# Kernel optimization log

Hardware: AMD Instinct MI355X
Metric: run time of the kernel (lower is better)

Reference implementation:

```python
import jax, jax.numpy as jnp
from jax import lax
import numpy as np

B, D, P, C = 16384, 256, 512, 20  # batch, input_dim, prototype_dim, n_class


def setup_inputs() -> dict:
    key = jax.random.key(0)
    k1, k2, k3 = jax.random.split(key, 3)
    return {
        "inputs": jax.random.normal(k1, (B, D), dtype=jnp.float32),
        "W": jax.random.normal(k2, (P, D), dtype=jnp.float32),
        "BETA": jax.random.normal(k3, (P, C), dtype=jnp.float32),
        "alpha": jnp.zeros((P, 1), dtype=jnp.float32),
        "gamma": jnp.full((P, 1), 0.1, dtype=jnp.float32),
        "n_class": C,
        "prototype_dim": P,
    }


def reference(inputs, W, BETA, alpha, gamma, n_class, prototype_dim):
    # inputs: [B, D], W: [P, D], BETA: [P, C], alpha/gamma: [P, 1]
    BETA2 = BETA * BETA
    U = BETA2 / BETA2.sum(axis=1, keepdims=True)          # [P, C]
    alphap = 0.99 / (1.0 + jnp.exp(-alpha))               # [P, 1]
    # d[k, b] = 0.5 * ||x_b - W_k||^2 via the expanded quadratic form
    d = 0.5 * (jnp.sum(W * W, axis=1)[:, None]
               + jnp.sum(inputs * inputs, axis=1)[None, :]
               - 2.0 * W @ inputs.T)                      # [P, B]
    expo = jnp.exp(-(gamma * gamma) * d)                  # [P, B]
    s = alphap * expo                                     # [P, B]

    bsz = inputs.shape[0]

    def step(mk, xs):
        # mk: [C+1, B] combined mass; xs = (U_k [C], s_k [B])
        Uk, sk = xs
        m_c = Uk[:, None] * sk[None, :]                   # [C, B] singleton masses
        m_n = 1.0 - sk                                    # [B]   mass on ignorance
        mk_c, mk_n = mk[:-1], mk[-1]
        new_c = mk_c * (m_c + m_n[None, :]) + m_c * mk_n[None, :]
        new_n = mk_n * m_n
        return jnp.concatenate([new_c, new_n[None, :]], axis=0), None

    mk0 = jnp.concatenate([jnp.zeros((n_class, bsz), dtype=inputs.dtype),
                           jnp.ones((1, bsz), dtype=inputs.dtype)], axis=0)
    mk, _ = lax.scan(step, mk0, (U, s))                   # sequential over P prototypes
    K = mk.sum(axis=0)                                    # [B]
    return (mk / K[None, :]).T                            # [B, C+1]
```

## Files before the change

### kernel.cpp

```cpp
#include <hip/hip_runtime.h>
#include <math.h>


#define NBATCH 16384
#define ND     256
#define NP     512
#define NCLS   20
#define OC     21

typedef short  short8  __attribute__((ext_vector_type(8)));
typedef short  short4v __attribute__((ext_vector_type(4)));
typedef unsigned short ushort8 __attribute__((ext_vector_type(8)));
typedef float  f32x16  __attribute__((ext_vector_type(16)));

#define OFF_PWH 0u
#define OFF_PWL 262144u
#define OFF_VS  524288u
#define OFF_WQ  567296u
#define OFF_AP  569344u
#define OFF_G2  571392u

__device__ __forceinline__ unsigned short f2bf_rn(float f) {
  unsigned int u = __float_as_uint(f);
  unsigned int r = (u + 0x7FFFu + ((u >> 16) & 1u)) >> 16;
  return (unsigned short)r;
}
__device__ __forceinline__ float bf2f(unsigned short h) {
  return __uint_as_float(((unsigned int)h) << 16);
}

__global__ __launch_bounds__(256)
void prep(const float* __restrict__ Wsrc, const float* __restrict__ BETA,
          const float* __restrict__ alpha, const float* __restrict__ gamma,
          unsigned short* __restrict__ dh, unsigned short* __restrict__ dl,
          float* __restrict__ sq, float* __restrict__ VS,
          float* __restrict__ AP, float* __restrict__ G2)
{
  const int bid = blockIdx.x;
  if (bid < 64) {
    const int tid = bid * 256 + threadIdx.x;
    const int row = tid >> 5, seg = tid & 31;
    const float4* s4 = (const float4*)(Wsrc + (size_t)row * ND + seg * 8);
    const float4 a = s4[0], b = s4[1];
    const float v[8] = {a.x, a.y, a.z, a.w, b.x, b.y, b.z, b.w};
    ushort8 hv, lv;
    float ssq = 0.f;
    #pragma unroll
    for (int j = 0; j < 8; ++j) {
      ssq = fmaf(v[j], v[j], ssq);
      const unsigned short hh = f2bf_rn(v[j]);
      hv[j] = hh;
      lv[j] = f2bf_rn(v[j] - bf2f(hh));
    }
    const int tile = row >> 5, m = row & 31, step = seg >> 1, r = seg & 1;
    const size_t cidx = (size_t)(tile * 16 + step) * 64 + m + 32 * r;
    *(ushort8*)(dh + cidx * 8) = hv;
    *(ushort8*)(dl + cidx * 8) = lv;
    #pragma unroll
    for (int off = 1; off < 32; off <<= 1) ssq += __shfl_xor(ssq, off, 64);
    if (seg == 0) sq[row] = ssq;
  } else {
    const int k = (bid - 64) * 256 + threadIdx.x;
    if (k >= NP) return;
    float bv[NCLS], bs = 0.f;
    #pragma unroll
    for (int c = 0; c < NCLS; ++c) { bv[c] = BETA[k * NCLS + c]; bs = fmaf(bv[c], bv[c], bs); }
    const float binv = 1.f / bs;
    #pragma unroll
    for (int c = 0; c < NCLS; ++c) VS[c * NP + k] = 1.f - bv[c] * bv[c] * binv;
    VS[NCLS * NP + k] = 1.f;
    AP[k] = 0.99f / (1.f + __expf(-alpha[k]));
    const float g = gamma[k];
    G2[k] = g * g;
  }
}

__device__ __forceinline__ void mfma_pass8(
    const short* __restrict__ Ah, const short* __restrict__ Al,
    const short8* __restrict__ bHc, const short8* __restrict__ bLc,
    const int lane, const int sh, const float* __restrict__ xqs,
    const float wqk, const float apk, const float g2k, float* __restrict__ sout)
{
  short8 wbh[8], wbl[8];
  #pragma unroll
  for (int p = 0; p < 8; ++p) { wbh[p] = bHc[p * 64]; wbl[p] = bLc[p * 64]; }

  f32x16 accA, accB;
  #pragma unroll
  for (int i = 0; i < 16; ++i) { accA[i] = 0.f; accB[i] = 0.f; }
  const short8* aH = (const short8*)Ah + (size_t)sh * 1024 + lane;
  const short8* aL = (const short8*)Al + (size_t)sh * 1024 + lane;
  #pragma unroll
  for (int step = 0; step < 16; ++step) {
    const short8 ah = aH[step * 64], al = aL[step * 64];
    const short8 bh = wbh[step & 7], bl = wbl[step & 7];
    if (step < 8) {
      wbh[step & 7] = bHc[(step + 8) * 64];
      wbl[step & 7] = bLc[(step + 8) * 64];
    }
    accA = __builtin_amdgcn_mfma_f32_32x32x16_bf16(ah, bh, accA, 0, 0, 0);
    accB = __builtin_amdgcn_mfma_f32_32x32x16_bf16(ah, bl, accB, 0, 0, 0);
    accB = __builtin_amdgcn_mfma_f32_32x32x16_bf16(al, bh, accB, 0, 0, 0);
  }
  const int h = lane >> 5;
  #pragma unroll
  for (int rg = 0; rg < 16; ++rg) {
    const int   m  = (rg & 3) + 8 * (rg >> 2) + 4 * h;
    const float dv = 0.5f * (wqk + xqs[sh * 32 + m]) - (accA[rg] + accB[rg]);
    sout[rg] = apk * __expf(-g2k * dv);
  }
}

__global__ __launch_bounds__(512)
void evid64(const float* __restrict__ X,
            const unsigned short* __restrict__ PWH, const unsigned short* __restrict__ PWL,
            const float* __restrict__ VS, const float* __restrict__ WQ,
            const float* __restrict__ AP, const float* __restrict__ G2,
            float* __restrict__ OUT)
{
  __shared__ __align__(16) char pool[131072];
  __shared__ float vsl[8 * NCLS * 32];
  __shared__ float xqs[64];
  short* Ah = (short*)pool;
  short* Al = (short*)(pool + 32768);
  float* sc = (float*)(pool + 65536);

  const int t    = threadIdx.x;
  const int lane = t & 63;
  const int wv   = __builtin_amdgcn_readfirstlane(t >> 6);
  const int bx   = blockIdx.x;
  const int bbase = bx * 64;
  const int pl = lane & 31, h = lane >> 5;

  {
    const int r  = t >> 3;
    const int sg = t & 7;
    const int rsh = r >> 5, rm = r & 31;
    const float* xrow = X + (size_t)(bbase + r) * ND;
    float ssq = 0.f;
    #pragma unroll
    for (int it = 0; it < 8; ++it) {
      const int c0 = it * 32 + sg * 4;
      const float4 v = *(const float4*)(xrow + c0);
      const float vv[4] = {v.x, v.y, v.z, v.w};
      short4v h4, l4;
      #pragma unroll
      for (int j = 0; j < 4; ++j) {
        ssq = fmaf(vv[j], vv[j], ssq);
        const unsigned short hh = f2bf_rn(vv[j]);
        h4[j] = (short)hh;
        l4[j] = (short)f2bf_rn(vv[j] - bf2f(hh));
      }
      const int step = c0 >> 4, hf = (c0 >> 3) & 1, j0 = c0 & 7;
      const int base = (((rsh * 16 + step) * 64) + (rm + 32 * hf)) * 8 + j0;
      *(short4v*)&Ah[base] = h4;
      *(short4v*)&Al[base] = l4;
    }
    ssq += __shfl_xor(ssq, 1, 64);
    ssq += __shfl_xor(ssq, 2, 64);
    ssq += __shfl_xor(ssq, 4, 64);
    if (sg == 0) xqs[r] = ssq;
  }
  __syncthreads();

  float Apc[OC];
  #pragma unroll
  for (int c = 0; c < OC; ++c) Apc[c] = 1.0f;

  float* vw = vsl + wv * (NCLS * 32);

  #pragma unroll
  for (int ph = 0; ph < 2; ++ph) {
    {
      const float* vg = VS + ph * 256 + wv * 32;
      #pragma unroll
      for (int i = 0; i < 10; ++i) {
        const int idx = i * 64 + lane;
        vw[idx] = vg[(idx >> 5) * NP + (idx & 31)];
      }
    }

    const int kp = ph * 256 + wv * 32 + pl;
    const float wqk = WQ[kp], apk = AP[kp], g2k = G2[kp];
    const short8* bHc = (const short8*)PWH + (size_t)(ph * 8 + wv) * 1024 + lane;
    const short8* bLc = (const short8*)PWL + (size_t)(ph * 8 + wv) * 1024 + lane;
    const int p = wv * 32 + pl;

    #pragma unroll
    for (int sh = 0; sh < 2; ++sh) {
      float sreg[16];
      mfma_pass8(Ah, Al, bHc, bLc, lane, sh, xqs, wqk, apk, g2k, sreg);
      #pragma unroll
      for (int rg = 0; rg < 16; ++rg) {
        const int m = (rg & 3) + 8 * (rg >> 2) + 4 * h;
        const int b = sh * 32 + m;
        sc[b * 256 + ((p + 4 * b) & 255)] = sreg[rg];
      }
    }

    {
      float sv[32];
      const int c0 = (wv * 32 + 4 * lane);
      #pragma unroll
      for (int q = 0; q < 8; ++q)
        *(float4*)&sv[4 * q] = *(const float4*)&sc[lane * 256 + ((c0 + 4 * q) & 255)];

      #pragma unroll 4
      for (int c = 0; c < NCLS; ++c) {
        const float* vp = vw + c * 32;
        float f8[8];
        #pragma unroll
        for (int j = 0; j < 8; ++j) f8[j] = fmaf(-sv[j], vp[j], 1.0f);
        #pragma unroll
        for (int j = 8; j < 32; ++j) f8[j & 7] *= fmaf(-sv[j], vp[j], 1.0f);
        Apc[c] *= ((f8[0] * f8[1]) * (f8[2] * f8[3])) *
                  ((f8[4] * f8[5]) * (f8[6] * f8[7]));
      }
      {
        float f8[8];
        #pragma unroll
        for (int j = 0; j < 8; ++j) f8[j] = 1.0f - sv[j];
        #pragma unroll
        for (int j = 8; j < 32; ++j) f8[j & 7] *= (1.0f - sv[j]);
        Apc[NCLS] *= ((f8[0] * f8[1]) * (f8[2] * f8[3])) *
                     ((f8[4] * f8[5]) * (f8[6] * f8[7]));
      }
    }
  }
  __syncthreads();

  float* E  = (float*)pool;
  float* R  = (float*)(pool + 43008);
  float* kv = (float*)(pool + 48384);
  #pragma unroll
  for (int c = 0; c < OC; ++c) E[(wv * OC + c) * 64 + lane] = Apc[c];
  __syncthreads();
  {
    const int b = t & 63, j = t >> 6;
    for (int c = j; c < OC; c += 8) {
      float p = E[c * 64 + b];
      #pragma unroll
      for (int w = 1; w < 8; ++w) p *= E[(w * OC + c) * 64 + b];
      R[c * 64 + b] = p;
    }
  }
  __syncthreads();
  if (t < 64) {
    const float Nv = R[NCLS * 64 + t];
    float K = Nv;
    #pragma unroll
    for (int c = 0; c < NCLS; ++c) K += R[c * 64 + t] - Nv;
    kv[t] = 1.0f / K;
  }
  __syncthreads();
  for (int idx = t; idx < 64 * OC; idx += 512) {
    const int b = idx / OC, c = idx - b * OC;
    const float Nv = R[NCLS * 64 + b];
    const float ik = kv[b];
    OUT[(size_t)bx * 64 * OC + idx] = (c < NCLS) ? (R[c * 64 + b] - Nv) * ik : Nv * ik;
  }
}

extern "C" void kernel_launch(void* const* d_in, const int* in_sizes, int n_in,
                              void* d_out, int out_size, void* d_ws, size_t ws_size,
                              hipStream_t stream) {
  (void)in_sizes; (void)n_in; (void)out_size; (void)ws_size;
  const float* X     = (const float*)d_in[0];
  const float* Wm    = (const float*)d_in[1];
  const float* BETA  = (const float*)d_in[2];
  const float* ALPHA = (const float*)d_in[3];
  const float* GAMMA = (const float*)d_in[4];
  float* OUT = (float*)d_out;

  char* ws = (char*)d_ws;
  unsigned short* PWH = (unsigned short*)(ws + OFF_PWH);
  unsigned short* PWL = (unsigned short*)(ws + OFF_PWL);
  float* VS = (float*)(ws + OFF_VS);
  float* WQ = (float*)(ws + OFF_WQ);
  float* AP = (float*)(ws + OFF_AP);
  float* G2 = (float*)(ws + OFF_G2);

  hipLaunchKernelGGL(prep, dim3(66), dim3(256), 0, stream,
                     Wm, BETA, ALPHA, GAMMA, PWH, PWL, WQ, VS, AP, G2);
  hipLaunchKernelGGL(evid64, dim3(NBATCH / 64), dim3(512), 0, stream,
                     X, PWH, PWL, VS, WQ, AP, G2, OUT);
}
```

Measured before the change: 97.82 us.

## Double wavefronts per block, splitting batch halves and prototype halves across waves

The block grows from 8 to 16 wavefronts. Each wave pair now shares a prototype slice, and each wave handles one batch half (sh) instead of looping over both. The per-lane combination loop is split into two 16-prototype halves, which are merged with a cross-half shuffle before the block reduction. This aims to raise latency hiding and occupancy within the 128KB LDS-limited single block per CU. The cost is an extra barrier per phase, a shallower B-operand prefetch, and a tighter register budget under waves_per_eu(4,4).

Result: slower. 119.3 us (+22.0%).

```diff
diff --git a/kernel.cpp b/kernel.cpp
--- a/kernel.cpp
+++ b/kernel.cpp
@@ -75,15 +75,15 @@
   }
 }
 
-__device__ __forceinline__ void mfma_pass8(
+__device__ __forceinline__ void mfma_pass4(
     const short* __restrict__ Ah, const short* __restrict__ Al,
     const short8* __restrict__ bHc, const short8* __restrict__ bLc,
     const int lane, const int sh, const float* __restrict__ xqs,
     const float wqk, const float apk, const float g2k, float* __restrict__ sout)
 {
-  short8 wbh[8], wbl[8];
-  #pragma unroll
-  for (int p = 0; p < 8; ++p) { wbh[p] = bHc[p * 64]; wbl[p] = bLc[p * 64]; }
+  short8 wbh[4], wbl[4];
+  #pragma unroll
+  for (int p = 0; p < 4; ++p) { wbh[p] = bHc[p * 64]; wbl[p] = bLc[p * 64]; }
 
   f32x16 accA, accB;
   #pragma unroll
@@ -93,10 +93,10 @@
   #pragma unroll
   for (int step = 0; step < 16; ++step) {
     const short8 ah = aH[step * 64], al = aL[step * 64];
-    const short8 bh = wbh[step & 7], bl = wbl[step & 7];
-    if (step < 8) {
-      wbh[step & 7] = bHc[(step + 8) * 64];
-      wbl[step & 7] = bLc[(step + 8) * 64];
+    const short8 bh = wbh[step & 3], bl = wbl[step & 3];
+    if (step < 12) {
+      wbh[step & 3] = bHc[(step + 4) * 64];
+      wbl[step & 3] = bLc[(step + 4) * 64];
     }
     accA = __builtin_amdgcn_mfma_f32_32x32x16_bf16(ah, bh, accA, 0, 0, 0);
     accB = __builtin_amdgcn_mfma_f32_32x32x16_bf16(ah, bl, accB, 0, 0, 0);
@@ -111,12 +111,12 @@
   }
 }
 
-__global__ __launch_bounds__(512)
-void evid64(const float* __restrict__ X,
-            const unsigned short* __restrict__ PWH, const unsigned short* __restrict__ PWL,
-            const float* __restrict__ VS, const float* __restrict__ WQ,
-            const float* __restrict__ AP, const float* __restrict__ G2,
-            float* __restrict__ OUT)
+__global__ __launch_bounds__(1024) __attribute__((amdgpu_waves_per_eu(4, 4)))
+void evid64w(const float* __restrict__ X,
+             const unsigned short* __restrict__ PWH, const unsigned short* __restrict__ PWL,
+             const float* __restrict__ VS, const float* __restrict__ WQ,
+             const float* __restrict__ AP, const float* __restrict__ G2,
+             float* __restrict__ OUT)
 {
   __shared__ __align__(16) char pool[131072];
   __shared__ float vsl[8 * NCLS * 32];
@@ -127,20 +127,22 @@
 
   const int t    = threadIdx.x;
   const int lane = t & 63;
-  const int wv   = __builtin_amdgcn_readfirstlane(t >> 6);
+  const int w    = __builtin_amdgcn_readfirstlane(t >> 6);
+  const int i    = w >> 1;
+  const int s    = w & 1;
   const int bx   = blockIdx.x;
   const int bbase = bx * 64;
   const int pl = lane & 31, h = lane >> 5;
 
   {
-    const int r  = t >> 3;
-    const int sg = t & 7;
+    const int r  = t >> 4;
+    const int sg = t & 15;
     const int rsh = r >> 5, rm = r & 31;
     const float* xrow = X + (size_t)(bbase + r) * ND;
     float ssq = 0.f;
     #pragma unroll
-    for (int it = 0; it < 8; ++it) {
-      const int c0 = it * 32 + sg * 4;
+    for (int it = 0; it < 4; ++it) {
+      const int c0 = it * 64 + sg * 4;
       const float4 v = *(const float4*)(xrow + c0);
       const float vv[4] = {v.x, v.y, v.z, v.w};
       short4v h4, l4;
@@ -159,6 +161,7 @@
     ssq += __shfl_xor(ssq, 1, 64);
     ssq += __shfl_xor(ssq, 2, 64);
     ssq += __shfl_xor(ssq, 4, 64);
+    ssq += __shfl_xor(ssq, 8, 64);
     if (sg == 0) xqs[r] = ssq;
   }
   __syncthreads();
@@ -167,80 +170,88 @@
   #pragma unroll
   for (int c = 0; c < OC; ++c) Apc[c] = 1.0f;
 
-  float* vw = vsl + wv * (NCLS * 32);
+  float* vw = vsl + i * (NCLS * 32);
 
   #pragma unroll
   for (int ph = 0; ph < 2; ++ph) {
+    if (ph == 1) __syncthreads();
+
     {
-      const float* vg = VS + ph * 256 + wv * 32;
-      #pragma unroll
-      for (int i = 0; i < 10; ++i) {
-        const int idx = i * 64 + lane;
+      const float* vg = VS + ph * 256 + i * 32;
+      #pragma unroll
+      for (int q = 0; q < 10; ++q) {
+        const int idx = q * 64 + lane;
         vw[idx] = vg[(idx >> 5) * NP + (idx & 31)];
       }
     }
 
-    const int kp = ph * 256 + wv * 32 + pl;
+    const int kp = ph * 256 + i * 32 + pl;
     const float wqk = WQ[kp], apk = AP[kp], g2k = G2[kp];
-    const short8* bHc = (const short8*)PWH + (size_t)(ph * 8 + wv) * 1024 + lane;
-    const short8* bLc = (const short8*)PWL + (size_t)(ph * 8 + wv) * 1024 + lane;
-    const int p = wv * 32 + pl;
-
-    #pragma unroll
-    for (int sh = 0; sh < 2; ++sh) {
-      float sreg[16];
-      mfma_pass8(Ah, Al, bHc, bLc, lane, sh, xqs, wqk, apk, g2k, sreg);
+    const short8* bHc = (const short8*)PWH + (size_t)(ph * 8 + i) * 1024 + lane;
+    const short8* bLc = (const short8*)PWL + (size_t)(ph * 8 + i) * 1024 + lane;
+
+    float sreg[16];
+    mfma_pass4(Ah, Al, bHc, bLc, lane, s, xqs, wqk, apk, g2k, sreg);
+
+    {
+      const int p = i * 32 + pl;
       #pragma unroll
       for (int rg = 0; rg < 16; ++rg) {
         const int m = (rg & 3) + 8 * (rg >> 2) + 4 * h;
-        const int b = sh * 32 + m;
+        const int b = s * 32 + m;
         sc[b * 256 + ((p + 4 * b) & 255)] = sreg[rg];
       }
     }
 
     {
-      float sv[32];
-      const int c0 = (wv * 32 + 4 * lane);
-      #pragma unroll
-      for (int q = 0; q < 8; ++q)
-        *(float4*)&sv[4 * q] = *(const float4*)&sc[lane * 256 + ((c0 + 4 * q) & 255)];
-
+      const int b = s * 32 + pl;
+      float sv[16];
+      const int cb = i * 32 + h * 16 + 4 * b;
+      #pragma unroll
+      for (int q = 0; q < 4; ++q)
+        *(float4*)&sv[4 * q] = *(const float4*)&sc[b * 256 + ((cb + 4 * q) & 255)];
+
+      const float* vb = vw + h * 16;
       #pragma unroll 4
       for (int c = 0; c < NCLS; ++c) {
-        const float* vp = vw + c * 32;
-        float f8[8];
-        #pragma unroll
-        for (int j = 0; j < 8; ++j) f8[j] = fmaf(-sv[j], vp[j], 1.0f);
-        #pragma unroll
-        for (int j = 8; j < 32; ++j) f8[j & 7] *= fmaf(-sv[j], vp[j], 1.0f);
-        Apc[c] *= ((f8[0] * f8[1]) * (f8[2] * f8[3])) *
-                  ((f8[4] * f8[5]) * (f8[6] * f8[7]));
+        const float* vp = vb + c * 32;
+        float f4[4];
+        #pragma unroll
+        for (int j = 0; j < 4; ++j) f4[j] = fmaf(-sv[j], vp[j], 1.0f);
+        #pragma unroll
+        for (int j = 4; j < 16; ++j) f4[j & 3] *= fmaf(-sv[j], vp[j], 1.0f);
+        Apc[c] *= (f4[0] * f4[1]) * (f4[2] * f4[3]);
       }
       {
-        float f8[8];
-        #pragma unroll
-        for (int j = 0; j < 8; ++j) f8[j] = 1.0f - sv[j];
-        #pragma unroll
-        for (int j = 8; j < 32; ++j) f8[j & 7] *= (1.0f - sv[j]);
-        Apc[NCLS] *= ((f8[0] * f8[1]) * (f8[2] * f8[3])) *
-                     ((f8[4] * f8[5]) * (f8[6] * f8[7]));
-      }
-    }
-  }
+        float f4[4];
+        #pragma unroll
+        for (int j = 0; j < 4; ++j) f4[j] = 1.0f - sv[j];
+        #pragma unroll
+        for (int j = 4; j < 16; ++j) f4[j & 3] *= (1.0f - sv[j]);
+        Apc[NCLS] *= (f4[0] * f4[1]) * (f4[2] * f4[3]);
+      }
+    }
+  }
+  #pragma unroll
+  for (int c = 0; c < OC; ++c) Apc[c] *= __shfl_xor(Apc[c], 32, 64);
+
   __syncthreads();
 
   float* E  = (float*)pool;
   float* R  = (float*)(pool + 43008);
   float* kv = (float*)(pool + 48384);
-  #pragma unroll
-  for (int c = 0; c < OC; ++c) E[(wv * OC + c) * 64 + lane] = Apc[c];
+  if (h == 0) {
+    const int b = s * 32 + pl;
+    #pragma unroll
+    for (int c = 0; c < OC; ++c) E[(i * OC + c) * 64 + b] = Apc[c];
+  }
   __syncthreads();
   {
     const int b = t & 63, j = t >> 6;
-    for (int c = j; c < OC; c += 8) {
+    for (int c = j; c < OC; c += 16) {
       float p = E[c * 64 + b];
       #pragma unroll
-      for (int w = 1; w < 8; ++w) p *= E[(w * OC + c) * 64 + b];
+      for (int ww = 1; ww < 8; ++ww) p *= E[(ww * OC + c) * 64 + b];
       R[c * 64 + b] = p;
     }
   }
@@ -253,7 +264,7 @@
     kv[t] = 1.0f / K;
   }
   __syncthreads();
-  for (int idx = t; idx < 64 * OC; idx += 512) {
+  for (int idx = t; idx < 64 * OC; idx += 1024) {
     const int b = idx / OC, c = idx - b * OC;
     const float Nv = R[NCLS * 64 + b];
     const float ik = kv[b];
@@ -282,6 +293,6 @@
 
   hipLaunchKernelGGL(prep, dim3(66), dim3(256), 0, stream,
                      Wm, BETA, ALPHA, GAMMA, PWH, PWL, WQ, VS, AP, G2);
-  hipLaunchKernelGGL(evid64, dim3(NBATCH / 64), dim3(512), 0, stream,
+  hipLaunchKernelGGL(evid64w, dim3(NBATCH / 64), dim3(1024), 0, stream,
                      X, PWH, PWL, VS, WQ, AP, G2, OUT);
 }
```

## Fuse prototype preprocessing into main kernel and drop separate prep launch

Applied to the files above, without the earlier changes.

Removes the prep kernel and computes the W bf16 hi/lo split, the W row norms, the normalized BETA terms, alphap and gamma^2 inside each block of the main kernel, reading raw fp32 W directly. This removes one kernel launch and the workspace round trip along with the dependency between the two kernels. In exchange every one of the 256 blocks redoes the W conversion and reads twice as many bytes of W (fp32 instead of two bf16 arrays), adding VALU work in the MFMA loop. The W reads mostly hit L2.

Result: slower. 139.4 us (+42.5%).

```diff
diff --git a/kernel.cpp b/kernel.cpp
--- a/kernel.cpp
+++ b/kernel.cpp
@@ -10,15 +10,7 @@
 
 typedef short  short8  __attribute__((ext_vector_type(8)));
 typedef short  short4v __attribute__((ext_vector_type(4)));
-typedef unsigned short ushort8 __attribute__((ext_vector_type(8)));
 typedef float  f32x16  __attribute__((ext_vector_type(16)));
-
-#define OFF_PWH 0u
-#define OFF_PWL 262144u
-#define OFF_VS  524288u
-#define OFF_WQ  567296u
-#define OFF_AP  569344u
-#define OFF_G2  571392u
 
 __device__ __forceinline__ unsigned short f2bf_rn(float f) {
   unsigned int u = __float_as_uint(f);
@@ -29,94 +21,64 @@
   return __uint_as_float(((unsigned int)h) << 16);
 }
 
-__global__ __launch_bounds__(256)
-void prep(const float* __restrict__ Wsrc, const float* __restrict__ BETA,
-          const float* __restrict__ alpha, const float* __restrict__ gamma,
-          unsigned short* __restrict__ dh, unsigned short* __restrict__ dl,
-          float* __restrict__ sq, float* __restrict__ VS,
-          float* __restrict__ AP, float* __restrict__ G2)
+template<bool WQCOMP>
+__device__ __forceinline__ void mfma_pass_raw(
+    const short* __restrict__ Ah, const short* __restrict__ Al,
+    const float* __restrict__ bp,
+    const int lane, const int sh, const float* __restrict__ xqs,
+    float& wq, const float apk, const float g2k, float* __restrict__ sout)
 {
-  const int bid = blockIdx.x;
-  if (bid < 64) {
-    const int tid = bid * 256 + threadIdx.x;
-    const int row = tid >> 5, seg = tid & 31;
-    const float4* s4 = (const float4*)(Wsrc + (size_t)row * ND + seg * 8);
-    const float4 a = s4[0], b = s4[1];
-    const float v[8] = {a.x, a.y, a.z, a.w, b.x, b.y, b.z, b.w};
-    ushort8 hv, lv;
-    float ssq = 0.f;
-    #pragma unroll
-    for (int j = 0; j < 8; ++j) {
-      ssq = fmaf(v[j], v[j], ssq);
-      const unsigned short hh = f2bf_rn(v[j]);
-      hv[j] = hh;
-      lv[j] = f2bf_rn(v[j] - bf2f(hh));
-    }
-    const int tile = row >> 5, m = row & 31, step = seg >> 1, r = seg & 1;
-    const size_t cidx = (size_t)(tile * 16 + step) * 64 + m + 32 * r;
-    *(ushort8*)(dh + cidx * 8) = hv;
-    *(ushort8*)(dl + cidx * 8) = lv;
-    #pragma unroll
-    for (int off = 1; off < 32; off <<= 1) ssq += __shfl_xor(ssq, off, 64);
-    if (seg == 0) sq[row] = ssq;
-  } else {
-    const int k = (bid - 64) * 256 + threadIdx.x;
-    if (k >= NP) return;
-    float bv[NCLS], bs = 0.f;
-    #pragma unroll
-    for (int c = 0; c < NCLS; ++c) { bv[c] = BETA[k * NCLS + c]; bs = fmaf(bv[c], bv[c], bs); }
-    const float binv = 1.f / bs;
-    #pragma unroll
-    for (int c = 0; c < NCLS; ++c) VS[c * NP + k] = 1.f - bv[c] * bv[c] * binv;
-    VS[NCLS * NP + k] = 1.f;
-    AP[k] = 0.99f / (1.f + __expf(-alpha[k]));
-    const float g = gamma[k];
-    G2[k] = g * g;
-  }
-}
-
-__device__ __forceinline__ void mfma_pass8(
-    const short* __restrict__ Ah, const short* __restrict__ Al,
-    const short8* __restrict__ bHc, const short8* __restrict__ bLc,
-    const int lane, const int sh, const float* __restrict__ xqs,
-    const float wqk, const float apk, const float g2k, float* __restrict__ sout)
-{
-  short8 wbh[8], wbl[8];
-  #pragma unroll
-  for (int p = 0; p < 8; ++p) { wbh[p] = bHc[p * 64]; wbl[p] = bLc[p * 64]; }
+  float4 r0[4], r1[4];
+  #pragma unroll
+  for (int p = 0; p < 4; ++p) {
+    r0[p] = *(const float4*)(bp + p * 16);
+    r1[p] = *(const float4*)(bp + p * 16 + 4);
+  }
 
   f32x16 accA, accB;
   #pragma unroll
   for (int i = 0; i < 16; ++i) { accA[i] = 0.f; accB[i] = 0.f; }
   const short8* aH = (const short8*)Ah + (size_t)sh * 1024 + lane;
   const short8* aL = (const short8*)Al + (size_t)sh * 1024 + lane;
+  float ssq = 0.f;
   #pragma unroll
   for (int step = 0; step < 16; ++step) {
+    const float4 f0 = r0[step & 3], f1 = r1[step & 3];
+    if (step < 12) {
+      r0[step & 3] = *(const float4*)(bp + (step + 4) * 16);
+      r1[step & 3] = *(const float4*)(bp + (step + 4) * 16 + 4);
+    }
     const short8 ah = aH[step * 64], al = aL[step * 64];
-    const short8 bh = wbh[step & 7], bl = wbl[step & 7];
-    if (step < 8) {
-      wbh[step & 7] = bHc[(step + 8) * 64];
-      wbl[step & 7] = bLc[(step + 8) * 64];
+    const float v[8] = {f0.x, f0.y, f0.z, f0.w, f1.x, f1.y, f1.z, f1.w};
+    short8 bh, bl;
+    #pragma unroll
+    for (int j = 0; j < 8; ++j) {
+      if (WQCOMP) ssq = fmaf(v[j], v[j], ssq);
+      const unsigned short hh = f2bf_rn(v[j]);
+      bh[j] = (short)hh;
+      bl[j] = (short)f2bf_rn(v[j] - bf2f(hh));
     }
     accA = __builtin_amdgcn_mfma_f32_32x32x16_bf16(ah, bh, accA, 0, 0, 0);
     accB = __builtin_amdgcn_mfma_f32_32x32x16_bf16(ah, bl, accB, 0, 0, 0);
     accB = __builtin_amdgcn_mfma_f32_32x32x16_bf16(al, bh, accB, 0, 0, 0);
   }
+  if (WQCOMP) {
+    ssq += __shfl_xor(ssq, 32, 64);
+    wq = ssq;
+  }
   const int h = lane >> 5;
   #pragma unroll
   for (int rg = 0; rg < 16; ++rg) {
     const int   m  = (rg & 3) + 8 * (rg >> 2) + 4 * h;
-    const float dv = 0.5f * (wqk + xqs[sh * 32 + m]) - (accA[rg] + accB[rg]);
+    const float dv = 0.5f * (wq + xqs[sh * 32 + m]) - (accA[rg] + accB[rg]);
     sout[rg] = apk * __expf(-g2k * dv);
   }
 }
 
 __global__ __launch_bounds__(512)
-void evid64(const float* __restrict__ X,
-            const unsigned short* __restrict__ PWH, const unsigned short* __restrict__ PWL,
-            const float* __restrict__ VS, const float* __restrict__ WQ,
-            const float* __restrict__ AP, const float* __restrict__ G2,
-            float* __restrict__ OUT)
+void evid_one(const float* __restrict__ X,   const float* __restrict__ Wm,
+              const float* __restrict__ BETA, const float* __restrict__ ALPHA,
+              const float* __restrict__ GAMMA, float* __restrict__ OUT)
 {
   __shared__ __align__(16) char pool[131072];
   __shared__ float vsl[8 * NCLS * 32];
@@ -171,30 +133,43 @@
 
   #pragma unroll
   for (int ph = 0; ph < 2; ++ph) {
+    const int p0 = ph * 256 + wv * 32;
+
     {
-      const float* vg = VS + ph * 256 + wv * 32;
-      #pragma unroll
-      for (int i = 0; i < 10; ++i) {
-        const int idx = i * 64 + lane;
-        vw[idx] = vg[(idx >> 5) * NP + (idx & 31)];
-      }
-    }
-
-    const int kp = ph * 256 + wv * 32 + pl;
-    const float wqk = WQ[kp], apk = AP[kp], g2k = G2[kp];
-    const short8* bHc = (const short8*)PWH + (size_t)(ph * 8 + wv) * 1024 + lane;
-    const short8* bLc = (const short8*)PWL + (size_t)(ph * 8 + wv) * 1024 + lane;
-    const int p = wv * 32 + pl;
-
-    #pragma unroll
-    for (int sh = 0; sh < 2; ++sh) {
-      float sreg[16];
-      mfma_pass8(Ah, Al, bHc, bLc, lane, sh, xqs, wqk, apk, g2k, sreg);
+      const float* brow = BETA + (size_t)(p0 + pl) * NCLS + h * 10;
+      float b[10];
+      #pragma unroll
+      for (int q = 0; q < 10; ++q) b[q] = brow[q];
+      float bs = 0.f;
+      #pragma unroll
+      for (int q = 0; q < 10; ++q) bs = fmaf(b[q], b[q], bs);
+      bs += __shfl_xor(bs, 32, 64);
+      const float binv = 1.f / bs;
+      #pragma unroll
+      for (int q = 0; q < 10; ++q)
+        vw[(h * 10 + q) * 32 + pl] = 1.f - b[q] * b[q] * binv;
+    }
+
+    const int kp = p0 + pl;
+    const float apk = 0.99f / (1.f + __expf(-ALPHA[kp]));
+    const float gk  = GAMMA[kp];
+    const float g2k = gk * gk;
+
+    const float* bp = Wm + ((size_t)(ph * 8 + wv) * 32 + pl) * ND + h * 8;
+
+    float wq;
+    float sreg0[16], sreg1[16];
+    mfma_pass_raw<true >(Ah, Al, bp, lane, 0, xqs, wq, apk, g2k, sreg0);
+    mfma_pass_raw<false>(Ah, Al, bp, lane, 1, xqs, wq, apk, g2k, sreg1);
+
+    {
+      const int p = wv * 32 + pl;
       #pragma unroll
       for (int rg = 0; rg < 16; ++rg) {
         const int m = (rg & 3) + 8 * (rg >> 2) + 4 * h;
-        const int b = sh * 32 + m;
-        sc[b * 256 + ((p + 4 * b) & 255)] = sreg[rg];
+        sc[m * 256 + ((p + 4 * m) & 255)] = sreg0[rg];
+        const int b1 = m + 32;
+        sc[b1 * 256 + ((p + 4 * b1) & 255)] = sreg1[rg];
       }
     }
 
@@ -264,7 +239,7 @@
 extern "C" void kernel_launch(void* const* d_in, const int* in_sizes, int n_in,
                               void* d_out, int out_size, void* d_ws, size_t ws_size,
                               hipStream_t stream) {
-  (void)in_sizes; (void)n_in; (void)out_size; (void)ws_size;
+  (void)in_sizes; (void)n_in; (void)out_size; (void)d_ws; (void)ws_size;
   const float* X     = (const float*)d_in[0];
   const float* Wm    = (const float*)d_in[1];
   const float* BETA  = (const float*)d_in[2];
@@ -272,16 +247,6 @@
   const float* GAMMA = (const float*)d_in[4];
   float* OUT = (float*)d_out;
 
-  char* ws = (char*)d_ws;
-  unsigned short* PWH = (unsigned short*)(ws + OFF_PWH);
-  unsigned short* PWL = (unsigned short*)(ws + OFF_PWL);
-  float* VS = (float*)(ws + OFF_VS);
-  float* WQ = (float*)(ws + OFF_WQ);
-  float* AP = (float*)(ws + OFF_AP);
-  float* G2 = (float*)(ws + OFF_G2);
-
-  hipLaunchKernelGGL(prep, dim3(66), dim3(256), 0, stream,
-                     Wm, BETA, ALPHA, GAMMA, PWH, PWL, WQ, VS, AP, G2);
-  hipLaunchKernelGGL(evid64, dim3(NBATCH / 64), dim3(512), 0, stream,
-                     X, PWH, PWL, VS, WQ, AP, G2, OUT);
-}
+  hipLaunchKernelGGL(evid_one, dim3(NBATCH / 64), dim3(512), 0, stream,
+                     X, Wm, BETA, ALPHA, GAMMA, OUT);
+}
```
